# Performance work log

Hardware: AMD Instinct MI355X
Metric: run time of the kernel (lower is better)

## Reference

```python
import jax, jax.numpy as jnp
import numpy as np

CROP = 14          # initial_crop_size
POOL_K = 2         # maxpool_kernel_size == maxpool_stride


def setup_inputs() -> dict:
    key = jax.random.key(0)
    k1, k2 = jax.random.split(key)
    features = jax.random.normal(k1, (1, 50, 50, 1024), dtype=jnp.float32)
    raw = jax.random.uniform(k2, (1, 300, 4), dtype=jnp.float32)
    # well-formed normalized boxes: y1<=y2, x1<=x2
    ys = jnp.sort(raw[..., 0::2], axis=-1)
    xs = jnp.sort(raw[..., 1::2], axis=-1)
    boxes = jnp.stack([ys[..., 0], xs[..., 0], ys[..., 1], xs[..., 1]], axis=-1)
    return {"features": features, "boxes": boxes}


def _crop_and_resize(feat, boxes, crop_size):
    # feat: [H, W, C]; boxes: [N, 4] normalized (y1, x1, y2, x2)
    # Matches tf.image.crop_and_resize bilinear semantics for crop_size > 1.
    H, W, _ = feat.shape
    y1, x1, y2, x2 = boxes[:, 0], boxes[:, 1], boxes[:, 2], boxes[:, 3]
    grid = jnp.arange(crop_size, dtype=feat.dtype)  # [S]
    # sample coordinates in source pixel space: [N, S]
    ys = y1[:, None] * (H - 1) + grid[None, :] * ((y2 - y1) * (H - 1) / (crop_size - 1))[:, None]
    xs = x1[:, None] * (W - 1) + grid[None, :] * ((x2 - x1) * (W - 1) / (crop_size - 1))[:, None]
    y0f = jnp.floor(ys)
    x0f = jnp.floor(xs)
    wy = (ys - y0f)[:, :, None, None]  # [N, S, 1, 1]
    wx = (xs - x0f)[:, None, :, None]  # [N, 1, S, 1]
    y0 = jnp.clip(y0f.astype(jnp.int32), 0, H - 1)
    y1i = jnp.clip(y0 + 1, 0, H - 1)
    x0 = jnp.clip(x0f.astype(jnp.int32), 0, W - 1)
    x1i = jnp.clip(x0 + 1, 0, W - 1)
    # four corner gathers -> [N, S, S, C]
    tl = feat[y0[:, :, None], x0[:, None, :]]
    tr = feat[y0[:, :, None], x1i[:, None, :]]
    bl = feat[y1i[:, :, None], x0[:, None, :]]
    br = feat[y1i[:, :, None], x1i[:, None, :]]
    top = tl + (tr - tl) * wx
    bot = bl + (br - bl) * wx
    return top + (bot - top) * wy


def reference(features, boxes):
    # features: [1, H, W, C]; boxes: [1, N, 4]
    crops = _crop_and_resize(features[0], boxes[0], CROP)  # [N, 14, 14, C]
    N, S, _, C = crops.shape
    P = S // POOL_K
    # 2x2 stride-2 max pool (kernel == stride, S even)
    pooled = crops.reshape(N, P, POOL_K, P, POOL_K, C).max(axis=(2, 4))  # [N, 7, 7, C]
    return pooled[None]  # [1, N, 7, 7, C]
```

## Files before the change

### kernel.cpp

```cpp
#include <hip/hip_runtime.h>
#include <math.h>

#define FH 50
#define FW 50
#define FC 1024
#define FC4 256
#define NBOX 300
#define PO 7
#define CHQ 4
#define NPIX (FH * FW * FC)
#define BF16_BYTES (NPIX * 2)

typedef float nat4 __attribute__((ext_vector_type(4)));

__device__ __forceinline__ nat4 lerp4(nat4 a, nat4 b, float w) {
    return a + (b - a) * w;
}
__device__ __forceinline__ nat4 max4(nat4 a, nat4 b) {
    nat4 r;
    r.x = fmaxf(a.x, b.x);
    r.y = fmaxf(a.y, b.y);
    r.z = fmaxf(a.z, b.z);
    r.w = fmaxf(a.w, b.w);
    return r;
}
__device__ __forceinline__ nat4 bf2f(uint2 u) {
    nat4 r;
    r.x = __uint_as_float(u.x << 16);
    r.y = __uint_as_float(u.x & 0xffff0000u);
    r.z = __uint_as_float(u.y << 16);
    r.w = __uint_as_float(u.y & 0xffff0000u);
    return r;
}
__device__ __forceinline__ unsigned bfpack(float a, float b) {
    unsigned ua = __float_as_uint(a);
    unsigned ub = __float_as_uint(b);
    ua += 0x7fffu + ((ua >> 16) & 1u);
    ub += 0x7fffu + ((ub >> 16) & 1u);
    return (ua >> 16) | (ub & 0xffff0000u);
}

__global__ __launch_bounds__(256) void cvt_kernel(
    const float* __restrict__ feat, unsigned* __restrict__ ws)
{
    const int i = blockIdx.x * 256 + threadIdx.x;
    const float4 v = reinterpret_cast<const float4*>(feat)[i];
    uint2 w;
    w.x = bfpack(v.x, v.y);
    w.y = bfpack(v.z, v.w);
    reinterpret_cast<uint2*>(ws)[i] = w;
}

__global__ __launch_bounds__(64) void roi_pool_bf16_kernel(
    const unsigned* __restrict__ ws,
    const float* __restrict__ boxes,
    float* __restrict__ out)
{
    const int j = blockIdx.x & 7;
    const int k = blockIdx.x >> 3;
    const int n = j + 8 * (k / (PO * CHQ));
    if (n >= NBOX) return;
    const int r  = k % (PO * CHQ);
    const int py = r >> 2;
    const int cq = r & 3;
    const int c  = cq * 64 + threadIdx.x;

    const float by1 = boxes[n * 4 + 0];
    const float bx1 = boxes[n * 4 + 1];
    const float by2 = boxes[n * 4 + 2];
    const float bx2 = boxes[n * 4 + 3];

    const float stepy = (by2 - by1) * (49.0f / 13.0f);
    const float stepx = (bx2 - bx1) * (49.0f / 13.0f);
    const float basey = by1 * 49.0f;
    const float basex = bx1 * 49.0f;

    const float ysA = basey + (float)(2 * py) * stepy;
    const float ysB = ysA + stepy;
    const float fA = floorf(ysA); const float wyA = ysA - fA;
    const float fB = floorf(ysB); const float wyB = ysB - fB;
    const int y0A = min(max((int)fA, 0), FH - 1); const int y1A = min(y0A + 1, FH - 1);
    const int y0B = min(max((int)fB, 0), FH - 1); const int y1B = min(y0B + 1, FH - 1);

    const uint2* __restrict__ f2 = reinterpret_cast<const uint2*>(ws);
    const int rA0 = y0A * FW, rA1 = y1A * FW, rB0 = y0B * FW, rB1 = y1B * FW;

    int cc = -1000;
    nat4 A00, A01, A10, A11, B00, B01, B10, B11;
    A00 = A01 = A10 = A11 = B00 = B01 = B10 = B11 = (nat4)0.0f;

    nat4 m = (nat4)(-INFINITY);
    nat4* __restrict__ obase =
        reinterpret_cast<nat4*>(out) + (size_t)(n * (PO * PO) + py * PO) * FC4 + c;

    for (int ix = 0; ix < 2 * PO; ++ix) {
        const float xs = basex + (float)ix * stepx;
        const float xf = floorf(xs);
        const float wx = xs - xf;
        int x0 = min(max((int)xf, 0), FW - 1);
        const int x1 = min(x0 + 1, FW - 1);

        if (x0 != cc) {
            if (x0 == cc + 1) {
                A00 = A01; A10 = A11; B00 = B01; B10 = B11;
                A01 = bf2f(f2[(rA0 + x1) * FC4 + c]);
                A11 = bf2f(f2[(rA1 + x1) * FC4 + c]);
                B01 = bf2f(f2[(rB0 + x1) * FC4 + c]);
                B11 = bf2f(f2[(rB1 + x1) * FC4 + c]);
            } else {
                A00 = bf2f(f2[(rA0 + x0) * FC4 + c]);
                A01 = bf2f(f2[(rA0 + x1) * FC4 + c]);
                A10 = bf2f(f2[(rA1 + x0) * FC4 + c]);
                A11 = bf2f(f2[(rA1 + x1) * FC4 + c]);
                B00 = bf2f(f2[(rB0 + x0) * FC4 + c]);
                B01 = bf2f(f2[(rB0 + x1) * FC4 + c]);
                B10 = bf2f(f2[(rB1 + x0) * FC4 + c]);
                B11 = bf2f(f2[(rB1 + x1) * FC4 + c]);
            }
            cc = x0;
        }

        const nat4 vA = lerp4(lerp4(A00, A01, wx), lerp4(A10, A11, wx), wyA);
        const nat4 vB = lerp4(lerp4(B00, B01, wx), lerp4(B10, B11, wx), wyB);
        m = max4(m, max4(vA, vB));

        if (ix & 1) {
            __builtin_nontemporal_store(m, obase + (ix >> 1) * FC4);
            m = (nat4)(-INFINITY);
        }
    }
}

__global__ __launch_bounds__(64) void roi_pool_f32_kernel(
    const float* __restrict__ feat,
    const float* __restrict__ boxes,
    float* __restrict__ out)
{
    const int j = blockIdx.x & 7;
    const int k = blockIdx.x >> 3;
    const int n = j + 8 * (k / (PO * CHQ));
    if (n >= NBOX) return;
    const int r  = k % (PO * CHQ);
    const int py = r >> 2;
    const int cq = r & 3;
    const int c4 = cq * 64 + threadIdx.x;

    const float by1 = boxes[n * 4 + 0];
    const float bx1 = boxes[n * 4 + 1];
    const float by2 = boxes[n * 4 + 2];
    const float bx2 = boxes[n * 4 + 3];
    const float stepy = (by2 - by1) * (49.0f / 13.0f);
    const float stepx = (bx2 - bx1) * (49.0f / 13.0f);
    const float basey = by1 * 49.0f;
    const float basex = bx1 * 49.0f;
    const float ysA = basey + (float)(2 * py) * stepy;
    const float ysB = ysA + stepy;
    const float fA = floorf(ysA); const float wyA = ysA - fA;
    const float fB = floorf(ysB); const float wyB = ysB - fB;
    const int y0A = min(max((int)fA, 0), FH - 1); const int y1A = min(y0A + 1, FH - 1);
    const int y0B = min(max((int)fB, 0), FH - 1); const int y1B = min(y0B + 1, FH - 1);

    const nat4* __restrict__ f4 = reinterpret_cast<const nat4*>(feat);
    const int rA0 = y0A * FW, rA1 = y1A * FW, rB0 = y0B * FW, rB1 = y1B * FW;

    int cc = -1000;
    nat4 A00, A01, A10, A11, B00, B01, B10, B11;
    A00 = A01 = A10 = A11 = B00 = B01 = B10 = B11 = (nat4)0.0f;
    nat4 m = (nat4)(-INFINITY);
    nat4* __restrict__ obase =
        reinterpret_cast<nat4*>(out) + (size_t)(n * (PO * PO) + py * PO) * FC4 + c4;

    for (int ix = 0; ix < 2 * PO; ++ix) {
        const float xs = basex + (float)ix * stepx;
        const float xf = floorf(xs);
        const float wx = xs - xf;
        int x0 = min(max((int)xf, 0), FW - 1);
        const int x1 = min(x0 + 1, FW - 1);
        if (x0 != cc) {
            if (x0 == cc + 1) {
                A00 = A01; A10 = A11; B00 = B01; B10 = B11;
                A01 = f4[(rA0 + x1) * FC4 + c4];
                A11 = f4[(rA1 + x1) * FC4 + c4];
                B01 = f4[(rB0 + x1) * FC4 + c4];
                B11 = f4[(rB1 + x1) * FC4 + c4];
            } else {
                A00 = f4[(rA0 + x0) * FC4 + c4];
                A01 = f4[(rA0 + x1) * FC4 + c4];
                A10 = f4[(rA1 + x0) * FC4 + c4];
                A11 = f4[(rA1 + x1) * FC4 + c4];
                B00 = f4[(rB0 + x0) * FC4 + c4];
                B01 = f4[(rB0 + x1) * FC4 + c4];
                B10 = f4[(rB1 + x0) * FC4 + c4];
                B11 = f4[(rB1 + x1) * FC4 + c4];
            }
            cc = x0;
        }
        const nat4 vA = lerp4(lerp4(A00, A01, wx), lerp4(A10, A11, wx), wyA);
        const nat4 vB = lerp4(lerp4(B00, B01, wx), lerp4(B10, B11, wx), wyB);
        m = max4(m, max4(vA, vB));
        if (ix & 1) {
            __builtin_nontemporal_store(m, obase + (ix >> 1) * FC4);
            m = (nat4)(-INFINITY);
        }
    }
}

extern "C" void kernel_launch(void* const* d_in, const int* in_sizes, int n_in,
                              void* d_out, int out_size, void* d_ws, size_t ws_size,
                              hipStream_t stream) {
    const float* feat  = (const float*)d_in[0];
    const float* boxes = (const float*)d_in[1];
    float* out = (float*)d_out;

    dim3 grid(8 * 38 * PO * CHQ);
    dim3 block(64);

    if (ws_size >= (size_t)BF16_BYTES) {
        unsigned* wsb = (unsigned*)d_ws;
        cvt_kernel<<<dim3(NPIX / 4 / 256), dim3(256), 0, stream>>>(feat, wsb);
        roi_pool_bf16_kernel<<<grid, block, 0, stream>>>(wsb, boxes, out);
    } else {
        roi_pool_f32_kernel<<<grid, block, 0, stream>>>(feat, boxes, out);
    }
}
```

Before: 99.09 us.

## Assign one pooled output cell per block with all gathers issued upfront

Measured after the change: 103.2 us. 4.2% more time.

```diff
diff --git a/kernel.cpp b/kernel.cpp
--- a/kernel.cpp
+++ b/kernel.cpp
@@ -7,7 +7,9 @@
 #define FC4 256
 #define NBOX 300
 #define PO 7
+#define NCELL (PO * PO)
 #define CHQ 4
+#define BPB (NCELL * CHQ)
 #define NPIX (FH * FW * FC)
 #define BF16_BYTES (NPIX * 2)
 
@@ -58,12 +60,14 @@
 {
     const int j = blockIdx.x & 7;
     const int k = blockIdx.x >> 3;
-    const int n = j + 8 * (k / (PO * CHQ));
+    const int n = j + 8 * (k / BPB);
     if (n >= NBOX) return;
-    const int r  = k % (PO * CHQ);
-    const int py = r >> 2;
-    const int cq = r & 3;
-    const int c  = cq * 64 + threadIdx.x;
+    const int rem  = k % BPB;
+    const int cell = rem >> 2;
+    const int cq   = rem & 3;
+    const int py   = cell / PO;
+    const int px   = cell - py * PO;
+    const int c    = cq * 64 + threadIdx.x;
 
     const float by1 = boxes[n * 4 + 0];
     const float bx1 = boxes[n * 4 + 1];
@@ -77,58 +81,50 @@
 
     const float ysA = basey + (float)(2 * py) * stepy;
     const float ysB = ysA + stepy;
-    const float fA = floorf(ysA); const float wyA = ysA - fA;
-    const float fB = floorf(ysB); const float wyB = ysB - fB;
-    const int y0A = min(max((int)fA, 0), FH - 1); const int y1A = min(y0A + 1, FH - 1);
-    const int y0B = min(max((int)fB, 0), FH - 1); const int y1B = min(y0B + 1, FH - 1);
+    const float xsL = basex + (float)(2 * px) * stepx;
+    const float xsR = xsL + stepx;
+
+    const float fyA = floorf(ysA); const float wyA = ysA - fyA;
+    const float fyB = floorf(ysB); const float wyB = ysB - fyB;
+    const float fxL = floorf(xsL); const float wxL = xsL - fxL;
+    const float fxR = floorf(xsR); const float wxR = xsR - fxR;
+
+    const int y0A = min(max((int)fyA, 0), FH - 1); const int y1A = min(y0A + 1, FH - 1);
+    const int y0B = min(max((int)fyB, 0), FH - 1); const int y1B = min(y0B + 1, FH - 1);
+    const int x0L = min(max((int)fxL, 0), FW - 1); const int x1L = min(x0L + 1, FW - 1);
+    const int x0R = min(max((int)fxR, 0), FW - 1); const int x1R = min(x0R + 1, FW - 1);
 
     const uint2* __restrict__ f2 = reinterpret_cast<const uint2*>(ws);
-    const int rA0 = y0A * FW, rA1 = y1A * FW, rB0 = y0B * FW, rB1 = y1B * FW;
-
-    int cc = -1000;
-    nat4 A00, A01, A10, A11, B00, B01, B10, B11;
-    A00 = A01 = A10 = A11 = B00 = B01 = B10 = B11 = (nat4)0.0f;
-
+    const int ry[4] = { y0A * FW, y1A * FW, y0B * FW, y1B * FW };
+    const int cx[4] = { x0L, x1L, x0R, x1R };
+
+    uint2 v[4][4];
+    #pragma unroll
+    for (int r = 0; r < 4; ++r)
+        #pragma unroll
+        for (int q = 0; q < 4; ++q)
+            v[r][q] = f2[(ry[r] + cx[q]) * FC4 + c];
+
+    const float wys[2] = { wyA, wyB };
+    const float wxs[2] = { wxL, wxR };
     nat4 m = (nat4)(-INFINITY);
-    nat4* __restrict__ obase =
-        reinterpret_cast<nat4*>(out) + (size_t)(n * (PO * PO) + py * PO) * FC4 + c;
-
-    for (int ix = 0; ix < 2 * PO; ++ix) {
-        const float xs = basex + (float)ix * stepx;
-        const float xf = floorf(xs);
-        const float wx = xs - xf;
-        int x0 = min(max((int)xf, 0), FW - 1);
-        const int x1 = min(x0 + 1, FW - 1);
-
-        if (x0 != cc) {
-            if (x0 == cc + 1) {
-                A00 = A01; A10 = A11; B00 = B01; B10 = B11;
-                A01 = bf2f(f2[(rA0 + x1) * FC4 + c]);
-                A11 = bf2f(f2[(rA1 + x1) * FC4 + c]);
-                B01 = bf2f(f2[(rB0 + x1) * FC4 + c]);
-                B11 = bf2f(f2[(rB1 + x1) * FC4 + c]);
-            } else {
-                A00 = bf2f(f2[(rA0 + x0) * FC4 + c]);
-                A01 = bf2f(f2[(rA0 + x1) * FC4 + c]);
-                A10 = bf2f(f2[(rA1 + x0) * FC4 + c]);
-                A11 = bf2f(f2[(rA1 + x1) * FC4 + c]);
-                B00 = bf2f(f2[(rB0 + x0) * FC4 + c]);
-                B01 = bf2f(f2[(rB0 + x1) * FC4 + c]);
-                B10 = bf2f(f2[(rB1 + x0) * FC4 + c]);
-                B11 = bf2f(f2[(rB1 + x1) * FC4 + c]);
-            }
-            cc = x0;
-        }
-
-        const nat4 vA = lerp4(lerp4(A00, A01, wx), lerp4(A10, A11, wx), wyA);
-        const nat4 vB = lerp4(lerp4(B00, B01, wx), lerp4(B10, B11, wx), wyB);
-        m = max4(m, max4(vA, vB));
-
-        if (ix & 1) {
-            __builtin_nontemporal_store(m, obase + (ix >> 1) * FC4);
-            m = (nat4)(-INFINITY);
+    #pragma unroll
+    for (int dy = 0; dy < 2; ++dy) {
+        #pragma unroll
+        for (int dx = 0; dx < 2; ++dx) {
+            const nat4 tl = bf2f(v[2 * dy    ][2 * dx]);
+            const nat4 tr = bf2f(v[2 * dy    ][2 * dx + 1]);
+            const nat4 bl = bf2f(v[2 * dy + 1][2 * dx]);
+            const nat4 br = bf2f(v[2 * dy + 1][2 * dx + 1]);
+            const nat4 s = lerp4(lerp4(tl, tr, wxs[dx]),
+                                 lerp4(bl, br, wxs[dx]), wys[dy]);
+            m = max4(m, s);
         }
     }
+
+    nat4* __restrict__ o4 = reinterpret_cast<nat4*>(out)
+                          + (size_t)(n * NCELL + cell) * FC4 + c;
+    __builtin_nontemporal_store(m, o4);
 }
 
 __global__ __launch_bounds__(64) void roi_pool_f32_kernel(
@@ -138,12 +134,14 @@
 {
     const int j = blockIdx.x & 7;
     const int k = blockIdx.x >> 3;
-    const int n = j + 8 * (k / (PO * CHQ));
+    const int n = j + 8 * (k / BPB);
     if (n >= NBOX) return;
-    const int r  = k % (PO * CHQ);
-    const int py = r >> 2;
-    const int cq = r & 3;
-    const int c4 = cq * 64 + threadIdx.x;
+    const int rem  = k % BPB;
+    const int cell = rem >> 2;
+    const int cq   = rem & 3;
+    const int py   = cell / PO;
+    const int px   = cell - py * PO;
+    const int c    = cq * 64 + threadIdx.x;
 
     const float by1 = boxes[n * 4 + 0];
     const float bx1 = boxes[n * 4 + 1];
@@ -155,54 +153,46 @@
     const float basex = bx1 * 49.0f;
     const float ysA = basey + (float)(2 * py) * stepy;
     const float ysB = ysA + stepy;
-    const float fA = floorf(ysA); const float wyA = ysA - fA;
-    const float fB = floorf(ysB); const float wyB = ysB - fB;
-    const int y0A = min(max((int)fA, 0), FH - 1); const int y1A = min(y0A + 1, FH - 1);
-    const int y0B = min(max((int)fB, 0), FH - 1); const int y1B = min(y0B + 1, FH - 1);
+    const float xsL = basex + (float)(2 * px) * stepx;
+    const float xsR = xsL + stepx;
+    const float fyA = floorf(ysA); const float wyA = ysA - fyA;
+    const float fyB = floorf(ysB); const float wyB = ysB - fyB;
+    const float fxL = floorf(xsL); const float wxL = xsL - fxL;
+    const float fxR = floorf(xsR); const float wxR = xsR - fxR;
+    const int y0A = min(max((int)fyA, 0), FH - 1); const int y1A = min(y0A + 1, FH - 1);
+    const int y0B = min(max((int)fyB, 0), FH - 1); const int y1B = min(y0B + 1, FH - 1);
+    const int x0L = min(max((int)fxL, 0), FW - 1); const int x1L = min(x0L + 1, FW - 1);
+    const int x0R = min(max((int)fxR, 0), FW - 1); const int x1R = min(x0R + 1, FW - 1);
 
     const nat4* __restrict__ f4 = reinterpret_cast<const nat4*>(feat);
-    const int rA0 = y0A * FW, rA1 = y1A * FW, rB0 = y0B * FW, rB1 = y1B * FW;
-
-    int cc = -1000;
-    nat4 A00, A01, A10, A11, B00, B01, B10, B11;
-    A00 = A01 = A10 = A11 = B00 = B01 = B10 = B11 = (nat4)0.0f;
+    const int ry[4] = { y0A * FW, y1A * FW, y0B * FW, y1B * FW };
+    const int cx[4] = { x0L, x1L, x0R, x1R };
+
+    nat4 v[4][4];
+    #pragma unroll
+    for (int r = 0; r < 4; ++r)
+        #pragma unroll
+        for (int q = 0; q < 4; ++q)
+            v[r][q] = f4[(ry[r] + cx[q]) * FC4 + c];
+
+    const float wys[2] = { wyA, wyB };
+    const float wxs[2] = { wxL, wxR };
     nat4 m = (nat4)(-INFINITY);
-    nat4* __restrict__ obase =
-        reinterpret_cast<nat4*>(out) + (size_t)(n * (PO * PO) + py * PO) * FC4 + c4;
-
-    for (int ix = 0; ix < 2 * PO; ++ix) {
-        const float xs = basex + (float)ix * stepx;
-        const float xf = floorf(xs);
-        const float wx = xs - xf;
-        int x0 = min(max((int)xf, 0), FW - 1);
-        const int x1 = min(x0 + 1, FW - 1);
-        if (x0 != cc) {
-            if (x0 == cc + 1) {
-                A00 = A01; A10 = A11; B00 = B01; B10 = B11;
-                A01 = f4[(rA0 + x1) * FC4 + c4];
-                A11 = f4[(rA1 + x1) * FC4 + c4];
-                B01 = f4[(rB0 + x1) * FC4 + c4];
-                B11 = f4[(rB1 + x1) * FC4 + c4];
-            } else {
-                A00 = f4[(rA0 + x0) * FC4 + c4];
-                A01 = f4[(rA0 + x1) * FC4 + c4];
-                A10 = f4[(rA1 + x0) * FC4 + c4];
-                A11 = f4[(rA1 + x1) * FC4 + c4];
-                B00 = f4[(rB0 + x0) * FC4 + c4];
-                B01 = f4[(rB0 + x1) * FC4 + c4];
-                B10 = f4[(rB1 + x0) * FC4 + c4];
-                B11 = f4[(rB1 + x1) * FC4 + c4];
-            }
-            cc = x0;
-        }
-        const nat4 vA = lerp4(lerp4(A00, A01, wx), lerp4(A10, A11, wx), wyA);
-        const nat4 vB = lerp4(lerp4(B00, B01, wx), lerp4(B10, B11, wx), wyB);
-        m = max4(m, max4(vA, vB));
-        if (ix & 1) {
-            __builtin_nontemporal_store(m, obase + (ix >> 1) * FC4);
-            m = (nat4)(-INFINITY);
+    #pragma unroll
+    for (int dy = 0; dy < 2; ++dy) {
+        #pragma unroll
+        for (int dx = 0; dx < 2; ++dx) {
+            const nat4 s = lerp4(
+                lerp4(v[2 * dy][2 * dx], v[2 * dy][2 * dx + 1], wxs[dx]),
+                lerp4(v[2 * dy + 1][2 * dx], v[2 * dy + 1][2 * dx + 1], wxs[dx]),
+                wys[dy]);
+            m = max4(m, s);
         }
     }
+
+    nat4* __restrict__ o4 = reinterpret_cast<nat4*>(out)
+                          + (size_t)(n * NCELL + cell) * FC4 + c;
+    __builtin_nontemporal_store(m, o4);
 }
 
 extern "C" void kernel_launch(void* const* d_in, const int* in_sizes, int n_in,
@@ -212,7 +202,7 @@
     const float* boxes = (const float*)d_in[1];
     float* out = (float*)d_out;
 
-    dim3 grid(8 * 38 * PO * CHQ);
+    dim3 grid(8 * 38 * BPB);
     dim3 block(64);
 
     if (ws_size >= (size_t)BF16_BYTES) {
```
